# Optimization experiments

Hardware: AMD Instinct MI355X
Metric: run time of the kernel (lower is better)

The kernel has to match this reference:

```python
import jax, jax.numpy as jnp
import numpy as np

B, C, H, W = 4, 256, 64, 64
N = H * W


def _conv1x1(x, w, b):
    # x: [B,C,H,W], w: [O,C], b: [O]  (1x1 conv == per-pixel linear)
    return jnp.einsum('bchw,oc->bohw', x, w) + b[None, :, None, None]


def setup_inputs() -> dict:
    key = jax.random.key(0)
    ks = jax.random.split(key, 11)
    s = 1.0 / np.sqrt(C)
    x = jax.random.normal(ks[0], (B, C, H, W), dtype=jnp.float32)
    mkw = lambda k: jax.random.normal(k, (C, C), dtype=jnp.float32) * s
    mkb = lambda k: jax.random.normal(k, (C,), dtype=jnp.float32) * 0.01
    return {
        'x': x,
        'w_teta': mkw(ks[1]), 'b_teta': mkb(ks[2]),
        'w_fi': mkw(ks[3]), 'b_fi': mkb(ks[4]),
        'w_gi': mkw(ks[5]), 'b_gi': mkb(ks[6]),
        'w_o1': mkw(ks[7]), 'b_o1': mkb(ks[8]),
        'w_o2': mkw(ks[9]), 'b_o2': mkb(ks[10]),
    }


def reference(x, w_teta, b_teta, w_fi, b_fi, w_gi, b_gi, w_o1, b_o1, w_o2, b_o2):
    b, c, h, w = x.shape
    n = h * w
    # 1x1 projections, flattened to [B,C,N]
    x1 = _conv1x1(x, w_teta, b_teta).reshape(b, c, n)
    x2 = _conv1x1(x, w_fi, b_fi).reshape(b, c, n)
    x3 = _conv1x1(x, w_gi, b_gi).reshape(b, c, n)
    # NOTE: original uses .view (memory reinterpretation), NOT transpose
    x1 = x1.reshape(b, n, c)
    x3 = x3.reshape(b, n, c)
    scores = jnp.einsum('bnc,bcm->bnm', x1, x2)      # [B,N,N]
    s_row = jax.nn.softmax(scores, axis=2)
    s_col = jax.nn.softmax(scores, axis=1)
    y1 = jnp.einsum('bnm,bmc->bnc', s_row, x3)       # [B,N,C]
    y2 = jnp.einsum('bnm,bmc->bnc', s_col, x3)
    # transpose(1,2) then view -> contiguous transpose + reshape
    y1 = jnp.swapaxes(y1, 1, 2).reshape(b, c, h, w)
    y2 = jnp.swapaxes(y2, 1, 2).reshape(b, c, h, w)
    o1 = _conv1x1(y1, w_o1, b_o1)
    o2 = _conv1x1(y2, w_o2, b_o2)
    xx = jnp.concatenate([x, x], axis=1)             # [B,2C,H,W]
    agg = jnp.concatenate([o1, o2], axis=1)
    return jax.nn.relu(xx + agg)
```

## Files before the change

kernel.cpp:

```cpp
#include <hip/hip_runtime.h>

#define BB   4
#define CC   256
#define NPIX 4096
#define AST2 40
#define YST  72

typedef __attribute__((ext_vector_type(8)))  short bf16x8;
typedef __attribute__((ext_vector_type(8)))  _Float16 f16x8;
typedef __attribute__((ext_vector_type(4)))  short short4v;
typedef __attribute__((ext_vector_type(16))) float f32x16;

__device__ __forceinline__ short f2h(float f) {
    _Float16 h = (_Float16)f;
    return __builtin_bit_cast(short, h);
}
__device__ __forceinline__ int cdrow(int r, int l5) {
    return (r & 3) + 8 * (r >> 2) + 4 * l5;
}
__device__ __forceinline__ short s_enc(float v) {
    float c = fmaxf(fminf(v, 127.9f), -127.9f);
    return (short)__float2int_rn(c * 256.0f);
}
__device__ __forceinline__ float s_dec(short v) {
    return (float)v * (1.0f / 256.0f);
}

__device__ __forceinline__ void mfma_core_f16(
    const short* __restrict__ A, const short* __restrict__ B, f32x16 acc[2][2])
{
    __shared__ short LA[128 * AST2], LB[128 * AST2];
    const int t = threadIdx.x;
    const int lane = t & 63, w = t >> 6;
    const int l31 = lane & 31, l5 = lane >> 5;
    const int nq = (w & 1) * 64, mq = (w >> 1) * 64;
    const int sr = t >> 1;
    const int sk = (t & 1) * 16;
    const size_t gs = (size_t)sr * 256 + sk;
    const int ls = sr * AST2 + sk;

    bf16x8 rA0 = *(const bf16x8*)(A + gs);
    bf16x8 rA1 = *(const bf16x8*)(A + gs + 8);
    bf16x8 rB0 = *(const bf16x8*)(B + gs);
    bf16x8 rB1 = *(const bf16x8*)(B + gs + 8);

    for (int k0 = 0; k0 < 256; k0 += 32) {
        __syncthreads();
        *(bf16x8*)&LA[ls]     = rA0;
        *(bf16x8*)&LA[ls + 8] = rA1;
        *(bf16x8*)&LB[ls]     = rB0;
        *(bf16x8*)&LB[ls + 8] = rB1;
        __syncthreads();
        if (k0 + 32 < 256) {
            size_t g = gs + k0 + 32;
            rA0 = *(const bf16x8*)(A + g);
            rA1 = *(const bf16x8*)(A + g + 8);
            rB0 = *(const bf16x8*)(B + g);
            rB1 = *(const bf16x8*)(B + g + 8);
        }
#pragma unroll
        for (int ks = 0; ks < 2; ks++) {
            f16x8 a[2], b[2];
#pragma unroll
            for (int s = 0; s < 2; s++) {
                a[s] = *(const f16x8*)&LA[(nq + s * 32 + l31) * AST2 + ks * 16 + l5 * 8];
                b[s] = *(const f16x8*)&LB[(mq + s * 32 + l31) * AST2 + ks * 16 + l5 * 8];
            }
#pragma unroll
            for (int s = 0; s < 2; s++)
#pragma unroll
                for (int u = 0; u < 2; u++)
                    acc[s][u] = __builtin_amdgcn_mfma_f32_32x32x16_f16(a[s], b[u], acc[s][u], 0, 0, 0);
        }
    }
}


__global__ __launch_bounds__(256) void pack_w5(
    const float* __restrict__ w0, const float* __restrict__ w1,
    const float* __restrict__ w2, const float* __restrict__ w3,
    const float* __restrict__ w4, short* __restrict__ wall)
{
    int which = blockIdx.y;
    const float* w = which == 0 ? w0 : which == 1 ? w1 : which == 2 ? w2
                   : which == 3 ? w3 : w4;
    int idx = blockIdx.x * 1024 + threadIdx.x * 4;
    float4 v = *(const float4*)(w + idx);
    short4v h;
    h.x = f2h(v.x); h.y = f2h(v.y); h.z = f2h(v.z); h.w = f2h(v.w);
    *(short4v*)(wall + which * 65536 + idx) = h;
}

__global__ __launch_bounds__(256) void pack_t_f16(
    const float* __restrict__ in, short* __restrict__ o16)
{
    __shared__ short T[32][36];
    const int b  = blockIdx.z;
    const int n0 = blockIdx.x * 32;
    const int c0 = blockIdx.y * 32;
    const float* src = in + (size_t)b * CC * NPIX;
    const int t = threadIdx.x;
    const int r = t >> 3, q = t & 7;
    float4 v = *(const float4*)(src + (size_t)(c0 + r) * NPIX + n0 + q * 4);
    T[q * 4 + 0][r] = f2h(v.x);
    T[q * 4 + 1][r] = f2h(v.y);
    T[q * 4 + 2][r] = f2h(v.z);
    T[q * 4 + 3][r] = f2h(v.w);
    __syncthreads();
    short4v o;
    o.x = T[r][q * 4 + 0];
    o.y = T[r][q * 4 + 1];
    o.z = T[r][q * 4 + 2];
    o.w = T[r][q * 4 + 3];
    size_t oo = (size_t)b * CC * NPIX + (size_t)(n0 + r) * 256 + c0 + q * 4;
    *(short4v*)(o16 + oo) = o;
}

__global__ __launch_bounds__(256) void tr16_cn(
    const short* __restrict__ in, short* __restrict__ outp)
{
    __shared__ short T[32][33];
    const int b  = blockIdx.z;
    const int n0 = blockIdx.x * 32;
    const int c0 = blockIdx.y * 32;
    const short* src = in + (size_t)b * CC * NPIX;
    short* dst = outp + (size_t)b * CC * NPIX;
    const int t = threadIdx.x;
    const int r = t >> 3, q = t & 7;
    short4v v = *(const short4v*)(src + (size_t)(c0 + r) * NPIX + n0 + q * 4);
    T[q * 4 + 0][r] = v.x;
    T[q * 4 + 1][r] = v.y;
    T[q * 4 + 2][r] = v.z;
    T[q * 4 + 3][r] = v.w;
    __syncthreads();
    short4v o;
    o.x = T[r][q * 4 + 0];
    o.y = T[r][q * 4 + 1];
    o.z = T[r][q * 4 + 2];
    o.w = T[r][q * 4 + 3];
    *(short4v*)(dst + (size_t)(n0 + r) * 256 + c0 + q * 4) = o;
}

__global__ __launch_bounds__(256) void packVt_bf(
    const short* __restrict__ x3f, short* __restrict__ Vt)
{
    __shared__ short T[32][33];
    const int b  = blockIdx.z;
    const int m0 = blockIdx.x * 32;
    const int c0 = blockIdx.y * 32;
    const short* in = x3f + (size_t)b * CC * NPIX;
    short* out = Vt + (size_t)b * CC * NPIX;
    const int t = threadIdx.x;
    const int r = t >> 3, q = t & 7;
    short4v v = *(const short4v*)(in + (size_t)(m0 + r) * CC + c0 + q * 4);
    T[q * 4 + 0][r] = v.x;
    T[q * 4 + 1][r] = v.y;
    T[q * 4 + 2][r] = v.z;
    T[q * 4 + 3][r] = v.w;
    __syncthreads();
    short4v o;
    o.x = T[r][q * 4 + 0];
    o.y = T[r][q * 4 + 1];
    o.z = T[r][q * 4 + 2];
    o.w = T[r][q * 4 + 3];
    *(short4v*)(out + (size_t)(c0 + r) * NPIX + m0 + q * 4) = o;
}


__global__ __launch_bounds__(256) void proj_mfma(
    const short* __restrict__ wpf, const short* __restrict__ xtf,
    const float* __restrict__ b_teta, const float* __restrict__ b_fi,
    const float* __restrict__ b_gi,
    short* __restrict__ x1f, short* __restrict__ x2f, short* __restrict__ x3f)
{
    const int z = blockIdx.z, p = z >> 2, b = z & 3;
    const int n0 = blockIdx.x * 128, c0 = blockIdx.y * 128;
    const size_t CN = (size_t)CC * NPIX;
    const short* Ah = wpf + p * 65536 + c0 * 256;
    const short* Bh = xtf + (size_t)b * CN + (size_t)n0 * 256;
    const float* bias = p == 0 ? b_teta : p == 1 ? b_fi : b_gi;
    short* dst = p == 0 ? x1f : p == 1 ? x2f : x3f;

    f32x16 acc[2][2] = {};
    mfma_core_f16(Ah, Bh, acc);

    const int t = threadIdx.x, lane = t & 63, w = t >> 6;
    const int l31 = lane & 31, l5 = lane >> 5;
    const int aq = (w & 1) * 64, bq = (w >> 1) * 64;
#pragma unroll
    for (int s = 0; s < 2; s++)
#pragma unroll
        for (int u = 0; u < 2; u++)
#pragma unroll
            for (int r = 0; r < 16; r++) {
                int c = c0 + aq + s * 32 + cdrow(r, l5);
                int n = n0 + bq + u * 32 + l31;
                float v = acc[s][u][r] + bias[c];
                size_t o = (size_t)b * CN + (size_t)c * NPIX + n;
                dst[o] = f2h(v);
            }
}

__global__ __launch_bounds__(256) void scores_mfma(
    const short* __restrict__ x1f, const short* __restrict__ x2tf,
    short* __restrict__ S16, float* __restrict__ pm, float* __restrict__ pl)
{
    const int m0 = blockIdx.x * 128, n0 = blockIdx.y * 128;
    f32x16 acc[2][2] = {};
    mfma_core_f16(x1f + (size_t)n0 * 256, x2tf + (size_t)m0 * 256, acc);

    const int t = threadIdx.x, lane = t & 63, w = t >> 6;
    const int l31 = lane & 31, l5 = lane >> 5;
    const int aq = (w & 1) * 64, bq = (w >> 1) * 64;
#pragma unroll
    for (int s = 0; s < 2; s++)
#pragma unroll
        for (int u = 0; u < 2; u++)
#pragma unroll
            for (int r = 0; r < 16; r++) {
                int n = n0 + aq + s * 32 + cdrow(r, l5);
                int m = m0 + bq + u * 32 + l31;
                S16[(size_t)n * NPIX + m] = s_enc(acc[s][u][r]);
            }

    const int member = w & 1;
#pragma unroll
    for (int u = 0; u < 2; u++) {
        float vmax = -1e30f;
#pragma unroll
        for (int s = 0; s < 2; s++)
#pragma unroll
            for (int r = 0; r < 16; r++) vmax = fmaxf(vmax, acc[s][u][r]);
        float vsum = 0.0f;
#pragma unroll
        for (int s = 0; s < 2; s++)
#pragma unroll
            for (int r = 0; r < 16; r++) vsum += __expf(acc[s][u][r] - vmax);
        float vmax2 = __shfl_xor(vmax, 32, 64);
        float vsum2 = __shfl_xor(vsum, 32, 64);
        float mc = fmaxf(vmax, vmax2);
        float sc = vsum * __expf(vmax - mc) + vsum2 * __expf(vmax2 - mc);
        if (l5 == 0) {
            size_t pidx = (size_t)(blockIdx.y * 2 + member) * NPIX + m0 + bq + u * 32 + l31;
            pm[pidx] = mc;
            pl[pidx] = sc;
        }
    }
}

__global__ __launch_bounds__(256) void out_mfma(
    const short* __restrict__ wof,
    const float* __restrict__ b_o1, const float* __restrict__ b_o2,
    const short* __restrict__ Yp,
    const float* __restrict__ x, float* __restrict__ out, int b)
{
    __shared__ short LA[128 * AST2], LB[128 * AST2];
    const size_t CN_ = (size_t)NPIX * CC;
    const int ch0 = blockIdx.y * 128;
    const int pix0 = blockIdx.x * 128;
    const int mode = ch0 < 256 ? 0 : 1;
    const short* W = wof + mode * 65536 + (size_t)(ch0 & 255) * 256;
    const short* Yq = Yp + (size_t)mode * 8 * CN_;
    const float* bias = mode == 0 ? b_o1 : b_o2;

    const int t = threadIdx.x, lane = t & 63, w = t >> 6;
    const int l31 = lane & 31, l5 = lane >> 5;
    const int nq = (w & 1) * 64, mq = (w >> 1) * 64;
    const int sr = t >> 1;
    const int sk = (t & 1) * 16;
    const size_t gsA = (size_t)sr * 256 + sk;
    const size_t gsB = (size_t)(pix0 + sr) * 256 + sk;
    const int ls = sr * AST2 + sk;

    f32x16 acc[2][2] = {};

    bf16x8 rA0 = *(const bf16x8*)(W + gsA);
    bf16x8 rA1 = *(const bf16x8*)(W + gsA + 8);
    f16x8 rB0, rB1;
    {
        rB0 = *(const f16x8*)(Yq + gsB);
        rB1 = *(const f16x8*)(Yq + gsB + 8);
#pragma unroll
        for (int q = 1; q < 8; q++) {
            rB0 = rB0 + *(const f16x8*)(Yq + (size_t)q * CN_ + gsB);
            rB1 = rB1 + *(const f16x8*)(Yq + (size_t)q * CN_ + gsB + 8);
        }
    }

    for (int k0 = 0; k0 < 256; k0 += 32) {
        __syncthreads();
        *(bf16x8*)&LA[ls]    = rA0;
        *(bf16x8*)&LA[ls + 8] = rA1;
        *(f16x8*)&LB[ls]     = rB0;
        *(f16x8*)&LB[ls + 8] = rB1;
        __syncthreads();
        if (k0 + 32 < 256) {
            size_t gA = gsA + k0 + 32;
            size_t gB = gsB + k0 + 32;
            rA0 = *(const bf16x8*)(W + gA);
            rA1 = *(const bf16x8*)(W + gA + 8);
            rB0 = *(const f16x8*)(Yq + gB);
            rB1 = *(const f16x8*)(Yq + gB + 8);
#pragma unroll
            for (int q = 1; q < 8; q++) {
                rB0 = rB0 + *(const f16x8*)(Yq + (size_t)q * CN_ + gB);
                rB1 = rB1 + *(const f16x8*)(Yq + (size_t)q * CN_ + gB + 8);
            }
        }
#pragma unroll
        for (int ks = 0; ks < 2; ks++) {
            f16x8 a[2], bb[2];
#pragma unroll
            for (int s = 0; s < 2; s++) {
                a[s]  = *(const f16x8*)&LA[(nq + s * 32 + l31) * AST2 + ks * 16 + l5 * 8];
                bb[s] = *(const f16x8*)&LB[(mq + s * 32 + l31) * AST2 + ks * 16 + l5 * 8];
            }
#pragma unroll
            for (int s = 0; s < 2; s++)
#pragma unroll
                for (int u = 0; u < 2; u++)
                    acc[s][u] = __builtin_amdgcn_mfma_f32_32x32x16_f16(a[s], bb[u], acc[s][u], 0, 0, 0);
        }
    }

    const int aq = (w & 1) * 64, bq = (w >> 1) * 64;
#pragma unroll
    for (int s = 0; s < 2; s++)
#pragma unroll
        for (int u = 0; u < 2; u++)
#pragma unroll
            for (int r = 0; r < 16; r++) {
                int ch = ch0 + aq + s * 32 + cdrow(r, l5);
                int pix = pix0 + bq + u * 32 + l31;
                int chm = ch & 255;
                float v = acc[s][u][r] + bias[chm] +
                          x[((size_t)b * CC + chm) * NPIX + pix];
                out[((size_t)b * 2 * CC + ch) * NPIX + pix] = fmaxf(v, 0.0f);
            }
}

__global__ __launch_bounds__(256) void stats16_kernel(
    const short* __restrict__ S16,
    const float* __restrict__ pm, const float* __restrict__ pl,
    float* __restrict__ cm, float* __restrict__ cli,
    float* __restrict__ rm, float* __restrict__ rli)
{
    __shared__ float sm[4][64], sl[4][64];
    __shared__ float red[4];
    const int t = threadIdx.x;
    if (blockIdx.x < 64) {
        const int cl = t & 63, ch = t >> 6;
        const int col = blockIdx.x * 64 + cl;
        float m = -1e30f, l = 0.0f;
        for (int i = ch * 16; i < ch * 16 + 16; i++) {
            float m2 = pm[(size_t)i * NPIX + col];
            float l2 = pl[(size_t)i * NPIX + col];
            float mn = fmaxf(m, m2);
            l = l * __expf(m - mn) + l2 * __expf(m2 - mn);
            m = mn;
        }
        sm[ch][cl] = m;
        sl[ch][cl] = l;
        __syncthreads();
        if (ch == 0) {
#pragma unroll
            for (int j = 1; j < 4; j++) {
                float m2 = sm[j][cl], l2 = sl[j][cl];
                float mn = fmaxf(m, m2);
                l = l * __expf(m - mn) + l2 * __expf(m2 - mn);
                m = mn;
            }
            cm[col]  = m;
            cli[col] = 1.0f / l;
        }
    } else {
        const int row = blockIdx.x - 64;
        const short* sp = S16 + (size_t)row * NPIX;
        const int w = t >> 6, lane = t & 63;
        float s4[16];
#pragma unroll
        for (int i = 0; i < 4; i++) {
            short4v v = *(const short4v*)(sp + (i * 256 + t) * 4);
            s4[i * 4 + 0] = s_dec(v.x);
            s4[i * 4 + 1] = s_dec(v.y);
            s4[i * 4 + 2] = s_dec(v.z);
            s4[i * 4 + 3] = s_dec(v.w);
        }
        float m = -1e30f;
#pragma unroll
        for (int i = 0; i < 16; i++) m = fmaxf(m, s4[i]);
        for (int off = 32; off; off >>= 1) m = fmaxf(m, __shfl_xor(m, off, 64));
        if (lane == 0) red[w] = m;
        __syncthreads();
        m = fmaxf(fmaxf(red[0], red[1]), fmaxf(red[2], red[3]));
        __syncthreads();
        float sum = 0.0f;
#pragma unroll
        for (int i = 0; i < 16; i++) sum += __expf(s4[i] - m);
        for (int off = 32; off; off >>= 1) sum += __shfl_xor(sum, off, 64);
        if (lane == 0) red[w] = sum;
        __syncthreads();
        if (t == 0) {
            rm[row]  = m;
            rli[row] = 1.0f / (red[0] + red[1] + red[2] + red[3]);
        }
    }
}

__global__ __launch_bounds__(256) void pv_kernel(
    const short* __restrict__ S16, const short* __restrict__ Vt,
    const float* __restrict__ rmv, const float* __restrict__ rliv,
    const float* __restrict__ cmv, const float* __restrict__ cliv,
    short* __restrict__ Yp)
{
    __shared__ short LA[64 * YST];
    __shared__ short LB[256 * YST];
    const int mode = blockIdx.z, kq = blockIdx.y;
    const int n0 = blockIdx.x * 64;
    const int kbase = kq * 512;

    const int t = threadIdx.x, lane = t & 63, w = t >> 6;
    const int l31 = lane & 31, l5 = lane >> 5;
    const int nst = (w & 1) * 32, cb = (w >> 1) * 128;
    const int ar = t >> 2;
    const int ak = (t & 3) * 16;

    const float mrow = rmv[n0 + ar];
    const float lrow = rliv[n0 + ar];
    const short* sp = S16 + (size_t)(n0 + ar) * NPIX + kbase + ak;

    short4v sv[4];
    bf16x8 pb[8];
#pragma unroll
    for (int i = 0; i < 4; i++)
        sv[i] = *(const short4v*)(sp + i * 4);
#pragma unroll
    for (int i = 0; i < 4; i++) {
        const short* bp = Vt + (size_t)(i * 64 + ar) * NPIX + kbase + ak;
        pb[2 * i]     = *(const bf16x8*)bp;
        pb[2 * i + 1] = *(const bf16x8*)(bp + 8);
    }

    f32x16 acc[4] = {};
    for (int s = 0; s < 8; s++) {
        short4v ph[4];
        if (mode == 0) {
#pragma unroll
            for (int i = 0; i < 4; i++) {
                ph[i].x = f2h(__expf(s_dec(sv[i].x) - mrow) * lrow);
                ph[i].y = f2h(__expf(s_dec(sv[i].y) - mrow) * lrow);
                ph[i].z = f2h(__expf(s_dec(sv[i].z) - mrow) * lrow);
                ph[i].w = f2h(__expf(s_dec(sv[i].w) - mrow) * lrow);
            }
        } else {
            const int mg = kbase + s * 64 + ak;
#pragma unroll
            for (int i = 0; i < 4; i++) {
                float4 cm4 = *(const float4*)(cmv + mg + i * 4);
                float4 cl4 = *(const float4*)(cliv + mg + i * 4);
                ph[i].x = f2h(__expf(s_dec(sv[i].x) - cm4.x) * cl4.x);
                ph[i].y = f2h(__expf(s_dec(sv[i].y) - cm4.y) * cl4.y);
                ph[i].z = f2h(__expf(s_dec(sv[i].z) - cm4.z) * cl4.z);
                ph[i].w = f2h(__expf(s_dec(sv[i].w) - cm4.w) * cl4.w);
            }
        }
        __syncthreads();
#pragma unroll
        for (int i = 0; i < 4; i++)
            *(short4v*)&LA[ar * YST + ak + i * 4] = ph[i];
#pragma unroll
        for (int i = 0; i < 4; i++) {
            *(bf16x8*)&LB[(i * 64 + ar) * YST + ak]     = pb[2 * i];
            *(bf16x8*)&LB[(i * 64 + ar) * YST + ak + 8] = pb[2 * i + 1];
        }
        __syncthreads();
        if (s + 1 < 8) {
            const short* spn = sp + (s + 1) * 64;
#pragma unroll
            for (int i = 0; i < 4; i++)
                sv[i] = *(const short4v*)(spn + i * 4);
            int kg = kbase + (s + 1) * 64 + ak;
#pragma unroll
            for (int i = 0; i < 4; i++) {
                const short* bp = Vt + (size_t)(i * 64 + ar) * NPIX + kg;
                pb[2 * i]     = *(const bf16x8*)bp;
                pb[2 * i + 1] = *(const bf16x8*)(bp + 8);
            }
        }
#pragma unroll
        for (int kc = 0; kc < 4; kc++) {
            f16x8 af = *(const f16x8*)&LA[(nst + l31) * YST + kc * 16 + l5 * 8];
#pragma unroll
            for (int u = 0; u < 4; u++) {
                f16x8 bf = *(const f16x8*)&LB[(cb + u * 32 + l31) * YST + kc * 16 + l5 * 8];
                acc[u] = __builtin_amdgcn_mfma_f32_32x32x16_f16(af, bf, acc[u], 0, 0, 0);
            }
        }
    }

    short* Yo = Yp + (size_t)(mode * 8 + kq) * ((size_t)NPIX * CC);
#pragma unroll
    for (int u = 0; u < 4; u++)
#pragma unroll
        for (int r = 0; r < 16; r++) {
            int rr = cdrow(r, l5);
            Yo[(size_t)(n0 + nst + rr) * CC + cb + u * 32 + l31] = f2h(acc[u][r]);
        }
}

extern "C" void kernel_launch(void* const* d_in, const int* in_sizes, int n_in,
                              void* d_out, int out_size, void* d_ws, size_t ws_size,
                              hipStream_t stream)
{
    (void)in_sizes; (void)n_in; (void)out_size; (void)ws_size;
    const float* x      = (const float*)d_in[0];
    const float* w_teta = (const float*)d_in[1];
    const float* b_teta = (const float*)d_in[2];
    const float* w_fi   = (const float*)d_in[3];
    const float* b_fi   = (const float*)d_in[4];
    const float* w_gi   = (const float*)d_in[5];
    const float* b_gi   = (const float*)d_in[6];
    const float* w_o1   = (const float*)d_in[7];
    const float* b_o1   = (const float*)d_in[8];
    const float* w_o2   = (const float*)d_in[9];
    const float* b_o2   = (const float*)d_in[10];
    float* out = (float*)d_out;

    const size_t CN = (size_t)CC * NPIX;
    const size_t NN = (size_t)NPIX * NPIX;
    short* wsp   = (short*)d_ws;
    short* S16   = wsp;
    short* Yp    = S16 + NN;
    short* x1f   = Yp + 16 * CN;
    short* x2tf  = x1f + BB * CN;
    short* Vtb   = x2tf + BB * CN;
    float* cm    = (float*)(Vtb + BB * CN);
    float* cli   = cm + NPIX;
    float* rm    = cli + NPIX;
    float* rli   = rm + NPIX;
    float* pm    = rli + NPIX;
    float* pl    = pm + 64 * NPIX;
    short* wall  = (short*)(pl + 64 * NPIX);
    short* wpf   = wall;
    short* wof   = wall + 3 * 65536;
    short* xtf  = Yp;
    short* x2f  = S16;
    short* x3f  = S16 + BB * CN;

    dim3 blk(256);
    pack_w5<<<dim3(64, 5), blk, 0, stream>>>(w_teta, w_fi, w_gi, w_o1, w_o2, wall);
    pack_t_f16<<<dim3(128, 8, 4), blk, 0, stream>>>(x, xtf);

    proj_mfma<<<dim3(32, 2, 12), blk, 0, stream>>>(
        wpf, xtf, b_teta, b_fi, b_gi, x1f, x2f, x3f);

    tr16_cn<<<dim3(128, 8, 4), blk, 0, stream>>>(x2f, x2tf);
    packVt_bf<<<dim3(128, 8, 4), blk, 0, stream>>>(x3f, Vtb);

    for (int b = 0; b < BB; b++) {
        scores_mfma<<<dim3(32, 32), blk, 0, stream>>>(
            x1f + b * CN, x2tf + b * CN, S16, pm, pl);
        stats16_kernel<<<dim3(64 + NPIX), blk, 0, stream>>>(
            S16, pm, pl, cm, cli, rm, rli);
        pv_kernel<<<dim3(64, 8, 2), blk, 0, stream>>>(
            S16, Vtb + b * CN, rm, rli, cm, cli, Yp);
        out_mfma<<<dim3(32, 4), blk, 0, stream>>>(
            wof, b_o1, b_o2, Yp, x, out, b);
    }
}
```

Before: 477.0 us.

## Use direct global-to-LDS loads in GEMM core and halve PV split-K

```diff
diff --git a/kernel.cpp b/kernel.cpp
--- a/kernel.cpp
+++ b/kernel.cpp
@@ -11,6 +11,13 @@
 typedef __attribute__((ext_vector_type(4)))  short short4v;
 typedef __attribute__((ext_vector_type(16))) float f32x16;
 
+typedef __attribute__((address_space(3))) unsigned int lds_u32;
+typedef __attribute__((address_space(1))) unsigned int gbl_u32;
+
+__device__ __forceinline__ void gl16(const short* g, short* l) {
+    __builtin_amdgcn_global_load_lds((gbl_u32*)g, (lds_u32*)l, 16, 0, 0);
+}
+
 __device__ __forceinline__ short f2h(float f) {
     _Float16 h = (_Float16)f;
     return __builtin_bit_cast(short, h);
@@ -26,38 +33,39 @@
     return (float)v * (1.0f / 256.0f);
 }
 
-__device__ __forceinline__ void mfma_core_f16(
+__device__ __forceinline__ void mfma_core_g16(
     const short* __restrict__ A, const short* __restrict__ B, f32x16 acc[2][2])
 {
     __shared__ short LA[128 * AST2], LB[128 * AST2];
     const int t = threadIdx.x;
-    const int lane = t & 63, w = t >> 6;
+    const int lane = t & 63, wv = t >> 6;
     const int l31 = lane & 31, l5 = lane >> 5;
-    const int nq = (w & 1) * 64, mq = (w >> 1) * 64;
-    const int sr = t >> 1;
-    const int sk = (t & 1) * 16;
-    const size_t gs = (size_t)sr * 256 + sk;
-    const int ls = sr * AST2 + sk;
-
-    bf16x8 rA0 = *(const bf16x8*)(A + gs);
-    bf16x8 rA1 = *(const bf16x8*)(A + gs + 8);
-    bf16x8 rB0 = *(const bf16x8*)(B + gs);
-    bf16x8 rB1 = *(const bf16x8*)(B + gs + 8);
+    const int nq = (wv & 1) * 64, mq = (wv >> 1) * 64;
+
+    int cbase[3];
+    int goff[3];
+    int cnum = 0;
+#pragma unroll
+    for (int j = 0; j < 3; j++) {
+        int ci = wv + j * 4;
+        if (ci < 10) {
+            int p = ci * 512 + lane * 8;
+            int row = p / AST2;
+            int kk = p - row * AST2;
+            if (kk >= 32) kk = 0;
+            cbase[cnum] = ci * 512;
+            goff[cnum] = row * 256 + kk;
+            cnum++;
+        }
+    }
 
     for (int k0 = 0; k0 < 256; k0 += 32) {
         __syncthreads();
-        *(bf16x8*)&LA[ls]     = rA0;
-        *(bf16x8*)&LA[ls + 8] = rA1;
-        *(bf16x8*)&LB[ls]     = rB0;
-        *(bf16x8*)&LB[ls + 8] = rB1;
-        __syncthreads();
-        if (k0 + 32 < 256) {
-            size_t g = gs + k0 + 32;
-            rA0 = *(const bf16x8*)(A + g);
-            rA1 = *(const bf16x8*)(A + g + 8);
-            rB0 = *(const bf16x8*)(B + g);
-            rB1 = *(const bf16x8*)(B + g + 8);
-        }
+        for (int j = 0; j < cnum; j++) {
+            gl16(A + goff[j] + k0, &LA[cbase[j]]);
+            gl16(B + goff[j] + k0, &LB[cbase[j]]);
+        }
+        __syncthreads();
 #pragma unroll
         for (int ks = 0; ks < 2; ks++) {
             f16x8 a[2], b[2];
@@ -182,7 +190,7 @@
     short* dst = p == 0 ? x1f : p == 1 ? x2f : x3f;
 
     f32x16 acc[2][2] = {};
-    mfma_core_f16(Ah, Bh, acc);
+    mfma_core_g16(Ah, Bh, acc);
 
     const int t = threadIdx.x, lane = t & 63, w = t >> 6;
     const int l31 = lane & 31, l5 = lane >> 5;
@@ -207,7 +215,7 @@
 {
     const int m0 = blockIdx.x * 128, n0 = blockIdx.y * 128;
     f32x16 acc[2][2] = {};
-    mfma_core_f16(x1f + (size_t)n0 * 256, x2tf + (size_t)m0 * 256, acc);
+    mfma_core_g16(x1f + (size_t)n0 * 256, x2tf + (size_t)m0 * 256, acc);
 
     const int t = threadIdx.x, lane = t & 63, w = t >> 6;
     const int l31 = lane & 31, l5 = lane >> 5;
@@ -260,7 +268,7 @@
     const int pix0 = blockIdx.x * 128;
     const int mode = ch0 < 256 ? 0 : 1;
     const short* W = wof + mode * 65536 + (size_t)(ch0 & 255) * 256;
-    const short* Yq = Yp + (size_t)mode * 8 * CN_;
+    const short* Yq = Yp + (size_t)mode * 4 * CN_;
     const float* bias = mode == 0 ? b_o1 : b_o2;
 
     const int t = threadIdx.x, lane = t & 63, w = t >> 6;
@@ -281,7 +289,7 @@
         rB0 = *(const f16x8*)(Yq + gsB);
         rB1 = *(const f16x8*)(Yq + gsB + 8);
 #pragma unroll
-        for (int q = 1; q < 8; q++) {
+        for (int q = 1; q < 4; q++) {
             rB0 = rB0 + *(const f16x8*)(Yq + (size_t)q * CN_ + gsB);
             rB1 = rB1 + *(const f16x8*)(Yq + (size_t)q * CN_ + gsB + 8);
         }
@@ -302,7 +310,7 @@
             rB0 = *(const f16x8*)(Yq + gB);
             rB1 = *(const f16x8*)(Yq + gB + 8);
 #pragma unroll
-            for (int q = 1; q < 8; q++) {
+            for (int q = 1; q < 4; q++) {
                 rB0 = rB0 + *(const f16x8*)(Yq + (size_t)q * CN_ + gB);
                 rB1 = rB1 + *(const f16x8*)(Yq + (size_t)q * CN_ + gB + 8);
             }
@@ -417,7 +425,7 @@
     __shared__ short LB[256 * YST];
     const int mode = blockIdx.z, kq = blockIdx.y;
     const int n0 = blockIdx.x * 64;
-    const int kbase = kq * 512;
+    const int kbase = kq * 1024;
 
     const int t = threadIdx.x, lane = t & 63, w = t >> 6;
     const int l31 = lane & 31, l5 = lane >> 5;
@@ -442,7 +450,7 @@
     }
 
     f32x16 acc[4] = {};
-    for (int s = 0; s < 8; s++) {
+    for (int s = 0; s < 16; s++) {
         short4v ph[4];
         if (mode == 0) {
 #pragma unroll
@@ -474,7 +482,7 @@
             *(bf16x8*)&LB[(i * 64 + ar) * YST + ak + 8] = pb[2 * i + 1];
         }
         __syncthreads();
-        if (s + 1 < 8) {
+        if (s + 1 < 16) {
             const short* spn = sp + (s + 1) * 64;
 #pragma unroll
             for (int i = 0; i < 4; i++)
@@ -498,7 +506,7 @@
         }
     }
 
-    short* Yo = Yp + (size_t)(mode * 8 + kq) * ((size_t)NPIX * CC);
+    short* Yo = Yp + (size_t)(mode * 4 + kq) * ((size_t)NPIX * CC);
 #pragma unroll
     for (int u = 0; u < 4; u++)
 #pragma unroll
@@ -562,7 +570,7 @@
             x1f + b * CN, x2tf + b * CN, S16, pm, pl);
         stats16_kernel<<<dim3(64 + NPIX), blk, 0, stream>>>(
             S16, pm, pl, cm, cli, rm, rli);
-        pv_kernel<<<dim3(64, 8, 2), blk, 0, stream>>>(
+        pv_kernel<<<dim3(64, 4, 2), blk, 0, stream>>>(
             S16, Vtb + b * CN, rm, rli, cm, cli, Yp);
         out_mfma<<<dim3(32, 4), blk, 0, stream>>>(
             wof, b_o1, b_o2, Yp, x, out, b);
```

Result: faster. 461.2 us (-3.3%).

## Halve PV split-K partitions and double-buffer register prefetch in pv_kernel

Applied to the files above, without the earlier changes.

```diff
diff --git a/kernel.cpp b/kernel.cpp
--- a/kernel.cpp
+++ b/kernel.cpp
@@ -260,7 +260,7 @@
     const int pix0 = blockIdx.x * 128;
     const int mode = ch0 < 256 ? 0 : 1;
     const short* W = wof + mode * 65536 + (size_t)(ch0 & 255) * 256;
-    const short* Yq = Yp + (size_t)mode * 8 * CN_;
+    const short* Yq = Yp + (size_t)mode * 4 * CN_;
     const float* bias = mode == 0 ? b_o1 : b_o2;
 
     const int t = threadIdx.x, lane = t & 63, w = t >> 6;
@@ -281,7 +281,7 @@
         rB0 = *(const f16x8*)(Yq + gsB);
         rB1 = *(const f16x8*)(Yq + gsB + 8);
 #pragma unroll
-        for (int q = 1; q < 8; q++) {
+        for (int q = 1; q < 4; q++) {
             rB0 = rB0 + *(const f16x8*)(Yq + (size_t)q * CN_ + gsB);
             rB1 = rB1 + *(const f16x8*)(Yq + (size_t)q * CN_ + gsB + 8);
         }
@@ -302,7 +302,7 @@
             rB0 = *(const f16x8*)(Yq + gB);
             rB1 = *(const f16x8*)(Yq + gB + 8);
 #pragma unroll
-            for (int q = 1; q < 8; q++) {
+            for (int q = 1; q < 4; q++) {
                 rB0 = rB0 + *(const f16x8*)(Yq + (size_t)q * CN_ + gB);
                 rB1 = rB1 + *(const f16x8*)(Yq + (size_t)q * CN_ + gB + 8);
             }
@@ -407,6 +407,32 @@
     }
 }
 
+__device__ __forceinline__ void compute_ph(
+    const short4v sv[4], int mode, int mg,
+    const float* __restrict__ cmv, const float* __restrict__ cliv,
+    float mrow, float lrow, short4v ph[4])
+{
+    if (mode == 0) {
+#pragma unroll
+        for (int i = 0; i < 4; i++) {
+            ph[i].x = f2h(__expf(s_dec(sv[i].x) - mrow) * lrow);
+            ph[i].y = f2h(__expf(s_dec(sv[i].y) - mrow) * lrow);
+            ph[i].z = f2h(__expf(s_dec(sv[i].z) - mrow) * lrow);
+            ph[i].w = f2h(__expf(s_dec(sv[i].w) - mrow) * lrow);
+        }
+    } else {
+#pragma unroll
+        for (int i = 0; i < 4; i++) {
+            float4 cm4 = *(const float4*)(cmv + mg + i * 4);
+            float4 cl4 = *(const float4*)(cliv + mg + i * 4);
+            ph[i].x = f2h(__expf(s_dec(sv[i].x) - cm4.x) * cl4.x);
+            ph[i].y = f2h(__expf(s_dec(sv[i].y) - cm4.y) * cl4.y);
+            ph[i].z = f2h(__expf(s_dec(sv[i].z) - cm4.z) * cl4.z);
+            ph[i].w = f2h(__expf(s_dec(sv[i].w) - cm4.w) * cl4.w);
+        }
+    }
+}
+
 __global__ __launch_bounds__(256) void pv_kernel(
     const short* __restrict__ S16, const short* __restrict__ Vt,
     const float* __restrict__ rmv, const float* __restrict__ rliv,
@@ -417,7 +443,7 @@
     __shared__ short LB[256 * YST];
     const int mode = blockIdx.z, kq = blockIdx.y;
     const int n0 = blockIdx.x * 64;
-    const int kbase = kq * 512;
+    const int kbase = kq * 1024;
 
     const int t = threadIdx.x, lane = t & 63, w = t >> 6;
     const int l31 = lane & 31, l5 = lane >> 5;
@@ -429,76 +455,100 @@
     const float lrow = rliv[n0 + ar];
     const short* sp = S16 + (size_t)(n0 + ar) * NPIX + kbase + ak;
 
-    short4v sv[4];
-    bf16x8 pb[8];
-#pragma unroll
-    for (int i = 0; i < 4; i++)
-        sv[i] = *(const short4v*)(sp + i * 4);
+    short4v svA[4], svB[4];
+    bf16x8 pbA[8], pbB[8];
 #pragma unroll
     for (int i = 0; i < 4; i++) {
-        const short* bp = Vt + (size_t)(i * 64 + ar) * NPIX + kbase + ak;
-        pb[2 * i]     = *(const bf16x8*)bp;
-        pb[2 * i + 1] = *(const bf16x8*)(bp + 8);
+        svA[i] = *(const short4v*)(sp + i * 4);
+        svB[i] = *(const short4v*)(sp + 64 + i * 4);
+    }
+#pragma unroll
+    for (int i = 0; i < 4; i++) {
+        const short* bp0 = Vt + (size_t)(i * 64 + ar) * NPIX + kbase + ak;
+        pbA[2 * i]     = *(const bf16x8*)bp0;
+        pbA[2 * i + 1] = *(const bf16x8*)(bp0 + 8);
+        pbB[2 * i]     = *(const bf16x8*)(bp0 + 64);
+        pbB[2 * i + 1] = *(const bf16x8*)(bp0 + 72);
     }
 
     f32x16 acc[4] = {};
-    for (int s = 0; s < 8; s++) {
-        short4v ph[4];
-        if (mode == 0) {
+    for (int sx = 0; sx < 8; sx++) {
+        const int s = sx * 2;
+        {
+            short4v ph[4];
+            compute_ph(svA, mode, kbase + s * 64 + ak, cmv, cliv, mrow, lrow, ph);
+            __syncthreads();
+#pragma unroll
+            for (int i = 0; i < 4; i++)
+                *(short4v*)&LA[ar * YST + ak + i * 4] = ph[i];
 #pragma unroll
             for (int i = 0; i < 4; i++) {
-                ph[i].x = f2h(__expf(s_dec(sv[i].x) - mrow) * lrow);
-                ph[i].y = f2h(__expf(s_dec(sv[i].y) - mrow) * lrow);
-                ph[i].z = f2h(__expf(s_dec(sv[i].z) - mrow) * lrow);
-                ph[i].w = f2h(__expf(s_dec(sv[i].w) - mrow) * lrow);
-            }
-        } else {
-            const int mg = kbase + s * 64 + ak;
+                *(bf16x8*)&LB[(i * 64 + ar) * YST + ak]     = pbA[2 * i];
+                *(bf16x8*)&LB[(i * 64 + ar) * YST + ak + 8] = pbA[2 * i + 1];
+            }
+            __syncthreads();
+            if (s + 2 < 16) {
+                const short* spn = sp + (s + 2) * 64;
+#pragma unroll
+                for (int i = 0; i < 4; i++)
+                    svA[i] = *(const short4v*)(spn + i * 4);
+                int kg = kbase + (s + 2) * 64 + ak;
+#pragma unroll
+                for (int i = 0; i < 4; i++) {
+                    const short* bp = Vt + (size_t)(i * 64 + ar) * NPIX + kg;
+                    pbA[2 * i]     = *(const bf16x8*)bp;
+                    pbA[2 * i + 1] = *(const bf16x8*)(bp + 8);
+                }
+            }
+#pragma unroll
+            for (int kc = 0; kc < 4; kc++) {
+                f16x8 af = *(const f16x8*)&LA[(nst + l31) * YST + kc * 16 + l5 * 8];
+#pragma unroll
+                for (int u = 0; u < 4; u++) {
+                    f16x8 bf = *(const f16x8*)&LB[(cb + u * 32 + l31) * YST + kc * 16 + l5 * 8];
+                    acc[u] = __builtin_amdgcn_mfma_f32_32x32x16_f16(af, bf, acc[u], 0, 0, 0);
+                }
+            }
+        }
+        {
+            short4v ph[4];
+            compute_ph(svB, mode, kbase + (s + 1) * 64 + ak, cmv, cliv, mrow, lrow, ph);
+            __syncthreads();
+#pragma unroll
+            for (int i = 0; i < 4; i++)
+                *(short4v*)&LA[ar * YST + ak + i * 4] = ph[i];
 #pragma unroll
             for (int i = 0; i < 4; i++) {
-                float4 cm4 = *(const float4*)(cmv + mg + i * 4);
-                float4 cl4 = *(const float4*)(cliv + mg + i * 4);
-                ph[i].x = f2h(__expf(s_dec(sv[i].x) - cm4.x) * cl4.x);
-                ph[i].y = f2h(__expf(s_dec(sv[i].y) - cm4.y) * cl4.y);
-                ph[i].z = f2h(__expf(s_dec(sv[i].z) - cm4.z) * cl4.z);
-                ph[i].w = f2h(__expf(s_dec(sv[i].w) - cm4.w) * cl4.w);
-            }
-        }
-        __syncthreads();
-#pragma unroll
-        for (int i = 0; i < 4; i++)
-            *(short4v*)&LA[ar * YST + ak + i * 4] = ph[i];
-#pragma unroll
-        for (int i = 0; i < 4; i++) {
-            *(bf16x8*)&LB[(i * 64 + ar) * YST + ak]     = pb[2 * i];
-            *(bf16x8*)&LB[(i * 64 + ar) * YST + ak + 8] = pb[2 * i + 1];
-        }
-        __syncthreads();
-        if (s + 1 < 8) {
-            const short* spn = sp + (s + 1) * 64;
-#pragma unroll
-            for (int i = 0; i < 4; i++)
-                sv[i] = *(const short4v*)(spn + i * 4);
-            int kg = kbase + (s + 1) * 64 + ak;
-#pragma unroll
-            for (int i = 0; i < 4; i++) {
-                const short* bp = Vt + (size_t)(i * 64 + ar) * NPIX + kg;
-                pb[2 * i]     = *(const bf16x8*)bp;
-                pb[2 * i + 1] = *(const bf16x8*)(bp + 8);
-            }
-        }
-#pragma unroll
-        for (int kc = 0; kc < 4; kc++) {
-            f16x8 af = *(const f16x8*)&LA[(nst + l31) * YST + kc * 16 + l5 * 8];
-#pragma unroll
-            for (int u = 0; u < 4; u++) {
-                f16x8 bf = *(const f16x8*)&LB[(cb + u * 32 + l31) * YST + kc * 16 + l5 * 8];
-                acc[u] = __builtin_amdgcn_mfma_f32_32x32x16_f16(af, bf, acc[u], 0, 0, 0);
-            }
-        }
-    }
-
-    short* Yo = Yp + (size_t)(mode * 8 + kq) * ((size_t)NPIX * CC);
+                *(bf16x8*)&LB[(i * 64 + ar) * YST + ak]     = pbB[2 * i];
+                *(bf16x8*)&LB[(i * 64 + ar) * YST + ak + 8] = pbB[2 * i + 1];
+            }
+            __syncthreads();
+            if (s + 3 < 16) {
+                const short* spn = sp + (s + 3) * 64;
+#pragma unroll
+                for (int i = 0; i < 4; i++)
+                    svB[i] = *(const short4v*)(spn + i * 4);
+                int kg = kbase + (s + 3) * 64 + ak;
+#pragma unroll
+                for (int i = 0; i < 4; i++) {
+                    const short* bp = Vt + (size_t)(i * 64 + ar) * NPIX + kg;
+                    pbB[2 * i]     = *(const bf16x8*)bp;
+                    pbB[2 * i + 1] = *(const bf16x8*)(bp + 8);
+                }
+            }
+#pragma unroll
+            for (int kc = 0; kc < 4; kc++) {
+                f16x8 af = *(const f16x8*)&LA[(nst + l31) * YST + kc * 16 + l5 * 8];
+#pragma unroll
+                for (int u = 0; u < 4; u++) {
+                    f16x8 bf = *(const f16x8*)&LB[(cb + u * 32 + l31) * YST + kc * 16 + l5 * 8];
+                    acc[u] = __builtin_amdgcn_mfma_f32_32x32x16_f16(af, bf, acc[u], 0, 0, 0);
+                }
+            }
+        }
+    }
+
+    short* Yo = Yp + (size_t)(mode * 4 + kq) * ((size_t)NPIX * CC);
 #pragma unroll
     for (int u = 0; u < 4; u++)
 #pragma unroll
@@ -562,7 +612,7 @@
             x1f + b * CN, x2tf + b * CN, S16, pm, pl);
         stats16_kernel<<<dim3(64 + NPIX), blk, 0, stream>>>(
             S16, pm, pl, cm, cli, rm, rli);
-        pv_kernel<<<dim3(64, 8, 2), blk, 0, stream>>>(
+        pv_kernel<<<dim3(64, 4, 2), blk, 0, stream>>>(
             S16, Vtb + b * CN, rm, rli, cm, cli, Yp);
         out_mfma<<<dim3(32, 4), blk, 0, stream>>>(
             wof, b_o1, b_o2, Yp, x, out, b);
```

Result: faster. 455.3 us (-4.5%).
